# Kernel tuning notes

Measured on AMD Instinct MI355X. Metric: run time of the kernel, lower is better.

Reference implementation:

```python
import jax, jax.numpy as jnp
import numpy as np

B, S, H = 64, 512, 1024  # batch, seq_len, hidden (input_size == hidden_size per source)


def setup_inputs() -> dict:
    key = jax.random.key(0)
    k1, k2 = jax.random.split(key)
    x = jax.random.normal(k1, (B, S, H), dtype=jnp.float32)
    # xavier_uniform_ for U: bound = sqrt(6/(fan_in+fan_out))
    bound = float(np.sqrt(6.0 / (H + 4 * H)))
    U = jax.random.uniform(k2, (H, 4 * H), dtype=jnp.float32, minval=-bound, maxval=bound)
    bias = jnp.zeros((4 * H,), dtype=jnp.float32)
    return {"x": x, "U": U, "bias": bias}


def reference(x, U, bias):
    # Faithful LSTM recurrence (peephole=False; note: W is declared in the
    # original module but never used in forward, and the gate matmul uses U
    # on the input x_t, exactly as in the source).
    batch = x.shape[0]
    HS = U.shape[0]
    h0 = jnp.zeros((batch, HS), dtype=x.dtype)
    c0 = jnp.zeros((batch, HS), dtype=x.dtype)

    def step(carry, x_t):
        h_t, c_t = carry
        gates = x_t @ U + bias  # [B, 4H]
        i_t = jax.nn.sigmoid(gates[:, :HS])
        f_t = jax.nn.sigmoid(gates[:, HS:2 * HS])
        g_t = jnp.tanh(gates[:, 2 * HS:3 * HS])
        o_t = jax.nn.sigmoid(gates[:, 3 * HS:])
        c_t = f_t * c_t + i_t * g_t
        h_t = o_t * jnp.tanh(c_t)
        return (h_t, c_t), h_t

    (h_T, c_T), hs = jax.lax.scan(step, (h0, c0), jnp.swapaxes(x, 0, 1))  # hs: [S, B, H]
    hidden_sequence = jnp.swapaxes(hs, 0, 1)  # [B, S, H]
    return hidden_sequence, (h_T, c_T)
```

## Files before the change

kernel.cpp:

```cpp
#include <hip/hip_runtime.h>
#include <hip/hip_bf16.h>
#include <stdint.h>

typedef __bf16 bf16x8 __attribute__((ext_vector_type(8)));
typedef float  f32x4  __attribute__((ext_vector_type(4)));
typedef unsigned short u16x8 __attribute__((ext_vector_type(8)));
typedef unsigned short u16x4 __attribute__((ext_vector_type(4)));
typedef _Float16 f16x4 __attribute__((ext_vector_type(4)));

#define HS    1024
#define FOURH 4096
#define SEQ   512
#define BATCH 64

#define BAR()  asm volatile("s_barrier" ::: "memory")
#define VMW(n) asm volatile("s_waitcnt vmcnt(" #n ")" ::: "memory")

__device__ __forceinline__ unsigned short f2bf(float f) {
    unsigned u = __builtin_bit_cast(unsigned, f);
    u = (u + 0x7FFFu + ((u >> 16) & 1u)) >> 16;
    return (unsigned short)u;
}

__device__ __forceinline__ void gload_lds16(const void* g, void* l) {
    __builtin_amdgcn_global_load_lds(
        (const __attribute__((address_space(1))) void*)g,
        (__attribute__((address_space(3))) void*)l, 16, 0, 0);
}

__device__ __forceinline__ float fsigmoid(float v) {
    return __builtin_amdgcn_rcpf(1.f + __expf(-v));
}
__device__ __forceinline__ float ftanh(float v) {
    return 1.f - 2.f * __builtin_amdgcn_rcpf(1.f + __expf(2.f * v));
}

__global__ __launch_bounds__(256) void convert_x(const float* __restrict__ x,
                                                 unsigned short* __restrict__ xb,
                                                 long n8) {
    long i = (long)blockIdx.x * blockDim.x + threadIdx.x;
    long stride = (long)gridDim.x * blockDim.x;
    for (; i < n8; i += stride) {
        const float4* p = (const float4*)(x + i * 8);
        float4 a = p[0], b = p[1];
        u16x8 o;
        o[0] = f2bf(a.x); o[1] = f2bf(a.y); o[2] = f2bf(a.z); o[3] = f2bf(a.w);
        o[4] = f2bf(b.x); o[5] = f2bf(b.y); o[6] = f2bf(b.z); o[7] = f2bf(b.w);
        *(u16x8*)(xb + i * 8) = o;
    }
}

__global__ __launch_bounds__(256) void transpose_u(const float* __restrict__ U,
                                                   unsigned short* __restrict__ Ut) {
    __shared__ float tile[32][33];
    int bx = blockIdx.x;
    int tn = bx >> 5;
    int tk = bx & 31;
    int c = threadIdx.x & 31;
    int r = threadIdx.x >> 5;
#pragma unroll
    for (int i = 0; i < 4; ++i) {
        int k = tk * 32 + r + i * 8;
        tile[r + i * 8][c] = U[(size_t)k * FOURH + tn * 32 + c];
    }
    __syncthreads();
#pragma unroll
    for (int i = 0; i < 4; ++i) {
        int nl = r + i * 8;
        Ut[(size_t)(tn * 32 + nl) * HS + tk * 32 + c] = f2bf(tile[c][nl]);
    }
}

__global__ __launch_bounds__(512, 1) void gemm_gates8(
    const unsigned short* __restrict__ Xb,
    const unsigned short* __restrict__ Ut,
    const float* __restrict__ bias,
    _Float16* __restrict__ gates,
    int lg2chunk, int s0) {
    __shared__ unsigned short LDSU[65536];

    int nwg = gridDim.x;
    int bid = blockIdx.x;
    int wg = (bid & 7) * (nwg >> 3) + (bid >> 3);
    int mt = wg >> 4;
    int nt = wg & 15;

    int tid = threadIdx.x;
    int w = tid >> 6, l = tid & 63;
    int wr = w >> 2, wc = w & 3;
    int lr = l & 15, lg = l >> 4;

    const int m0 = mt * 256, n0 = nt * 256;
    const int cmask = (1 << lg2chunk) - 1;

    const int rdo = lr * 32 + ((lg * 8) ^ ((lr & 8) << 1));

    const int srow = l >> 2;
    const int skin = ((l & 3) * 8) ^ (((l >> 5) & 1) << 4);

    const unsigned short* pAq[4];
    const unsigned short* pBq[4];
#pragma unroll
    for (int q = 0; q < 4; ++q) {
        int rowg = q * 64 + (w >> 1) * 16 + srow;
        int mrow = m0 + rowg;
        int b = mrow >> lg2chunk, sl2 = mrow & cmask;
        pAq[q] = Xb + (size_t)(b * SEQ + s0 + sl2) * HS + (w & 1) * 32 + skin;
        pBq[q] = Ut + (size_t)(n0 + rowg) * HS + (w & 1) * 32 + skin;
    }
    const int dsub = (w >> 1) * 2 + (w & 1);

    f32x4 acc[8][4];
#pragma unroll
    for (int mi = 0; mi < 8; ++mi)
#pragma unroll
        for (int ni = 0; ni < 4; ++ni) acc[mi][ni] = 0.f;

#define SA(T, Q) gload_lds16(pAq[Q] + (T) * 64, \
        &LDSU[(((T) & 1) << 15) + ((Q) * 8 + dsub) * 512])
#define SB(T, Q) gload_lds16(pBq[Q] + (T) * 64, \
        &LDSU[(((T) & 1) << 15) + 16384 + ((Q) * 8 + dsub) * 512])

    bf16x8 aq[2][4], bn0[2][2], bn1[2][2];

#define RDA(MH) \
    _Pragma("unroll") for (int ks = 0; ks < 2; ++ks) \
    _Pragma("unroll") for (int mi = 0; mi < 4; ++mi) \
        aq[ks][mi] = *(const bf16x8*)(buf + ((wr * 8 + (MH) * 4 + mi) * 2 + ks) * 512 + rdo)
#define RDB(NH, BN) \
    _Pragma("unroll") for (int ks = 0; ks < 2; ++ks) \
    _Pragma("unroll") for (int ni = 0; ni < 2; ++ni) \
        BN[ks][ni] = *(const bf16x8*)(buf + 16384 + ((wc * 4 + (NH) * 2 + ni) * 2 + ks) * 512 + rdo)
#define MMQ(MH, NH, BN) \
    __builtin_amdgcn_s_setprio(1); \
    _Pragma("unroll") for (int ks = 0; ks < 2; ++ks) \
    _Pragma("unroll") for (int mi = 0; mi < 4; ++mi) \
    _Pragma("unroll") for (int ni = 0; ni < 2; ++ni) \
        acc[(MH) * 4 + mi][(NH) * 2 + ni] = __builtin_amdgcn_mfma_f32_16x16x32_bf16( \
            aq[ks][mi], BN[ks][ni], acc[(MH) * 4 + mi][(NH) * 2 + ni], 0, 0, 0); \
    __builtin_amdgcn_s_setprio(0)

    SA(0, 0); SA(0, 2); SB(0, 0); SB(0, 1); SB(0, 2); SB(0, 3); SA(0, 1); SA(0, 3);
    VMW(2); BAR();

    for (int t = 0; t < 16; ++t) {
        const unsigned short* buf = &LDSU[(t & 1) << 15];
        RDA(0);
        RDB(0, bn0);
        if (t < 15) { SA(t + 1, 0); SA(t + 1, 2); }
        MMQ(0, 0, bn0);
        RDB(1, bn1);
        if (t < 15) { SB(t + 1, 0); SB(t + 1, 1); SB(t + 1, 2); SB(t + 1, 3); }
        MMQ(0, 1, bn1);
        if (t < 15) { VMW(6); } else { VMW(0); }
        BAR();
        RDA(1);
        if (t < 15) { SA(t + 1, 1); SA(t + 1, 3); }
        MMQ(1, 1, bn1);
        MMQ(1, 0, bn0);
        if (t < 15) { VMW(2); }
        BAR();
    }

#pragma unroll
    for (int ni = 0; ni < 4; ++ni) {
        int gcol = n0 + wc * 64 + ni * 16 + lr;
        bool is_g = ((gcol >> 10) == 2);
        float bv = bias[gcol];
#pragma unroll
        for (int mi = 0; mi < 8; ++mi) {
            int rg = ((m0 + wr * 128 + mi * 16) >> 2) + lg;
            u16x4 pk;
#pragma unroll
            for (int r = 0; r < 4; ++r) {
                float v = acc[mi][ni][r] + bv;
                float e = is_g ? ftanh(v) : fsigmoid(v);
                pk[r] = __builtin_bit_cast(unsigned short, (_Float16)e);
            }
            *(u16x4*)(gates + ((size_t)rg * FOURH + gcol) * 4) = pk;
        }
    }
#undef SA
#undef SB
#undef RDA
#undef RDB
#undef MMQ
}

__global__ __launch_bounds__(256) void lstm_recur(
    const _Float16* __restrict__ gates,
    float* __restrict__ out,
    float* __restrict__ cstate,
    int chunk, int s0) {
    int t = blockIdx.x * 256 + threadIdx.x;
    int b = t >> 10, h = t & 1023;
    float c = (s0 == 0) ? 0.f : cstate[t];
    const _Float16* gp = gates + ((size_t)((b * chunk) >> 2) * FOURH + h) * 4;
    float* op = out + (size_t)(b * SEQ + s0) * HS + h;
    float hv = 0.f;
    const int ng = chunk >> 2;
    for (int g4 = 0; g4 < ng; g4 += 2) {
        f16x4 iv[2], fv[2], gv[2], ov[2];
#pragma unroll
        for (int u = 0; u < 2; ++u) {
            const _Float16* q = gp + (size_t)(g4 + u) * (FOURH * 4);
            iv[u] = *(const f16x4*)(q);
            fv[u] = *(const f16x4*)(q + 4096);
            gv[u] = *(const f16x4*)(q + 8192);
            ov[u] = *(const f16x4*)(q + 12288);
        }
#pragma unroll
        for (int u = 0; u < 2; ++u) {
#pragma unroll
            for (int r = 0; r < 4; ++r) {
                c = (float)fv[u][r] * c + (float)iv[u][r] * (float)gv[u][r];
                float th = ftanh(c);
                hv = (float)ov[u][r] * th;
                op[(size_t)((g4 + u) * 4 + r) * HS] = hv;
            }
        }
    }
    cstate[t] = c;
    if (s0 + chunk == SEQ) {
        out[(size_t)BATCH * SEQ * HS + t] = hv;
        out[(size_t)BATCH * SEQ * HS + BATCH * HS + t] = c;
    }
}

extern "C" void kernel_launch(void* const* d_in, const int* in_sizes, int n_in,
                              void* d_out, int out_size, void* d_ws, size_t ws_size,
                              hipStream_t stream) {
    const float* x    = (const float*)d_in[0];
    const float* U    = (const float*)d_in[1];
    const float* bias = (const float*)d_in[2];
    float* out = (float*)d_out;
    char*  ws  = (char*)d_ws;

    unsigned short* Xb = (unsigned short*)ws;
    unsigned short* Ut = (unsigned short*)(ws + 67108864);
    float* cstate      = (float*)(ws + 75497472);
    _Float16* gates    = (_Float16*)(ws + 75759616);
    const size_t fixed = 75759616;

    int chunk = 512;
    while (chunk > 4 && fixed + (size_t)BATCH * chunk * FOURH * 2 > ws_size)
        chunk >>= 1;
    int lg2 = 31 - __builtin_clz(chunk);

    convert_x<<<2048, 256, 0, stream>>>(x, Xb, (long)BATCH * SEQ * HS / 8);
    transpose_u<<<4096, 256, 0, stream>>>(U, Ut);

    for (int s0 = 0; s0 < SEQ; s0 += chunk) {
        int mtiles = (BATCH * chunk) / 256;
        gemm_gates8<<<mtiles * 16, 512, 0, stream>>>(Xb, Ut, bias, gates, lg2, s0);
        lstm_recur<<<256, 256, 0, stream>>>(gates, out, cstate, chunk, s0);
    }
}
```

Measured before the change: 401.3 us.

## Stage LSTM recurrence gate loads through double-buffered LDS with async copies

Adds a recurrence kernel that prefetches the next 16 timesteps of gate values into a double-buffered LDS region using direct global-to-LDS loads. The element-wise recurrence then reads from LDS while the next block streams in, hiding the global load latency along the serial time loop. The fallback kernel drops its two-step unrolled prefetch. The cost is extra barriers and 64KB of LDS per block, which limits occupancy.

```diff
diff --git a/kernel.cpp b/kernel.cpp
--- a/kernel.cpp
+++ b/kernel.cpp
@@ -94,7 +94,6 @@
     const int cmask = (1 << lg2chunk) - 1;
 
     const int rdo = lr * 32 + ((lg * 8) ^ ((lr & 8) << 1));
-
     const int srow = l >> 2;
     const int skin = ((l & 3) * 8) ^ (((l >> 5) & 1) << 4);
 
@@ -187,10 +186,74 @@
 #undef MMQ
 }
 
-__global__ __launch_bounds__(256) void lstm_recur(
+__global__ __launch_bounds__(256) void lstm_recur_lds(
     const _Float16* __restrict__ gates,
     float* __restrict__ out,
     float* __restrict__ cstate,
+    int chunk, int s0) {
+    __shared__ unsigned char LB[2][32768];
+
+    int tid = threadIdx.x;
+    int b = blockIdx.x >> 2;
+    int h0 = (blockIdx.x & 3) * 256;
+    int h = h0 + tid;
+    int tg = b * HS + h;
+
+    float c = (s0 == 0) ? 0.f : cstate[tg];
+    float hv = 0.f;
+    const size_t rgbase = (size_t)(b * chunk) >> 2;
+    const char* gbase = (const char*)gates;
+    float* op = out + (size_t)(b * SEQ + s0) * HS + h;
+
+    const int M = chunk >> 4;
+    const int wbase = (tid & 0xC0) * 16;
+
+    auto STAGE = [&](int m) {
+        unsigned char* dst0 = &LB[m & 1][0];
+        size_t rg0 = rgbase + (size_t)m * 4;
+#pragma unroll
+        for (int j = 0; j < 8; ++j) {
+            int q = j * 256 + tid;
+            int stripe = q >> 7;
+            int u = q & 127;
+            const char* src = gbase +
+                ((rg0 + (stripe >> 2)) * FOURH + (stripe & 3) * 1024 + h0 + u * 2) * 8;
+            gload_lds16(src, dst0 + j * 4096 + wbase);
+        }
+    };
+
+    STAGE(0);
+    for (int m = 0; m < M; ++m) {
+        if (m + 1 < M) { STAGE(m + 1); VMW(8); }
+        else           { VMW(0); }
+        BAR();
+        const unsigned char* sb = &LB[m & 1][0];
+#pragma unroll
+        for (int rg = 0; rg < 4; ++rg) {
+            f16x4 iv = *(const f16x4*)(sb + ((rg * 4 + 0) * 2048) + tid * 8);
+            f16x4 fv = *(const f16x4*)(sb + ((rg * 4 + 1) * 2048) + tid * 8);
+            f16x4 gv = *(const f16x4*)(sb + ((rg * 4 + 2) * 2048) + tid * 8);
+            f16x4 ov = *(const f16x4*)(sb + ((rg * 4 + 3) * 2048) + tid * 8);
+#pragma unroll
+            for (int r = 0; r < 4; ++r) {
+                c = (float)fv[r] * c + (float)iv[r] * (float)gv[r];
+                float th = ftanh(c);
+                hv = (float)ov[r] * th;
+                op[(size_t)(m * 16 + rg * 4 + r) * HS] = hv;
+            }
+        }
+        BAR();
+    }
+    cstate[tg] = c;
+    if (s0 + chunk == SEQ) {
+        out[(size_t)BATCH * SEQ * HS + tg] = hv;
+        out[(size_t)BATCH * SEQ * HS + BATCH * HS + tg] = c;
+    }
+}
+
+__global__ __launch_bounds__(256) void lstm_recur(
+    const _Float16* __restrict__ gates,
+    float* __restrict__ out, float* __restrict__ cstate,
     int chunk, int s0) {
     int t = blockIdx.x * 256 + threadIdx.x;
     int b = t >> 10, h = t & 1023;
@@ -199,25 +262,18 @@
     float* op = out + (size_t)(b * SEQ + s0) * HS + h;
     float hv = 0.f;
     const int ng = chunk >> 2;
-    for (int g4 = 0; g4 < ng; g4 += 2) {
-        f16x4 iv[2], fv[2], gv[2], ov[2];
-#pragma unroll
-        for (int u = 0; u < 2; ++u) {
-            const _Float16* q = gp + (size_t)(g4 + u) * (FOURH * 4);
-            iv[u] = *(const f16x4*)(q);
-            fv[u] = *(const f16x4*)(q + 4096);
-            gv[u] = *(const f16x4*)(q + 8192);
-            ov[u] = *(const f16x4*)(q + 12288);
-        }
-#pragma unroll
-        for (int u = 0; u < 2; ++u) {
-#pragma unroll
-            for (int r = 0; r < 4; ++r) {
-                c = (float)fv[u][r] * c + (float)iv[u][r] * (float)gv[u][r];
-                float th = ftanh(c);
-                hv = (float)ov[u][r] * th;
-                op[(size_t)((g4 + u) * 4 + r) * HS] = hv;
-            }
+    for (int g4 = 0; g4 < ng; ++g4) {
+        const _Float16* q = gp + (size_t)g4 * (FOURH * 4);
+        f16x4 iv = *(const f16x4*)(q);
+        f16x4 fv = *(const f16x4*)(q + 4096);
+        f16x4 gv = *(const f16x4*)(q + 8192);
+        f16x4 ov = *(const f16x4*)(q + 12288);
+#pragma unroll
+        for (int r = 0; r < 4; ++r) {
+            c = (float)fv[r] * c + (float)iv[r] * (float)gv[r];
+            float th = ftanh(c);
+            hv = (float)ov[r] * th;
+            op[(size_t)(g4 * 4 + r) * HS] = hv;
         }
     }
     cstate[t] = c;
@@ -253,6 +309,9 @@
     for (int s0 = 0; s0 < SEQ; s0 += chunk) {
         int mtiles = (BATCH * chunk) / 256;
         gemm_gates8<<<mtiles * 16, 512, 0, stream>>>(Xb, Ut, bias, gates, lg2, s0);
-        lstm_recur<<<256, 256, 0, stream>>>(gates, out, cstate, chunk, s0);
-    }
-}
+        if ((chunk & 15) == 0)
+            lstm_recur_lds<<<256, 256, 0, stream>>>(gates, out, cstate, chunk, s0);
+        else
+            lstm_recur<<<256, 256, 0, stream>>>(gates, out, cstate, chunk, s0);
+    }
+}
```

After: 400.5 us. Within noise of the previous version (-0.2%).

## Interleave U columns by gate so GEMM epilogue fuses i*g product

Applied to the files above, without the earlier changes.

The transposed weight rows are permuted so that each 16-column group of a wave holds the same hidden units across all four gates. The GEMM epilogue can then compute i*g, f and o together and store only three fp16 gate planes instead of four. This cuts the gate intermediate's write and read traffic by a quarter and lets a larger chunk fit in the workspace. The recurrence kernel reads the three planes and gains a remainder loop for odd group counts.

```diff
diff --git a/kernel.cpp b/kernel.cpp
--- a/kernel.cpp
+++ b/kernel.cpp
@@ -67,7 +67,10 @@
 #pragma unroll
     for (int i = 0; i < 4; ++i) {
         int nl = r + i * 8;
-        Ut[(size_t)(tn * 32 + nl) * HS + tk * 32 + c] = f2bf(tile[c][nl]);
+        int n = tn * 32 + nl;
+        int gate = n >> 10, h = n & 1023;
+        int pn = ((h >> 4) << 6) | (gate << 4) | (h & 15);
+        Ut[(size_t)pn * HS + tk * 32 + c] = f2bf(tile[c][nl]);
     }
 }
 
@@ -94,7 +97,6 @@
     const int cmask = (1 << lg2chunk) - 1;
 
     const int rdo = lr * 32 + ((lg * 8) ^ ((lr & 8) << 1));
-
     const int srow = l >> 2;
     const int skin = ((l & 3) * 8) ^ (((l >> 5) & 1) << 4);
 
@@ -162,23 +164,28 @@
         BAR();
     }
 
-#pragma unroll
-    for (int ni = 0; ni < 4; ++ni) {
-        int gcol = n0 + wc * 64 + ni * 16 + lr;
-        bool is_g = ((gcol >> 10) == 2);
-        float bv = bias[gcol];
-#pragma unroll
-        for (int mi = 0; mi < 8; ++mi) {
-            int rg = ((m0 + wr * 128 + mi * 16) >> 2) + lg;
-            u16x4 pk;
-#pragma unroll
-            for (int r = 0; r < 4; ++r) {
-                float v = acc[mi][ni][r] + bv;
-                float e = is_g ? ftanh(v) : fsigmoid(v);
-                pk[r] = __builtin_bit_cast(unsigned short, (_Float16)e);
-            }
-            *(u16x4*)(gates + ((size_t)rg * FOURH + gcol) * 4) = pk;
-        }
+    const int hh = ((n0 >> 6) + wc) * 16 + lr;
+    const float bi = bias[hh], bf = bias[1024 + hh];
+    const float bg = bias[2048 + hh], bo = bias[3072 + hh];
+#pragma unroll
+    for (int mi = 0; mi < 8; ++mi) {
+        size_t rg = (size_t)(((m0 + wr * 128 + mi * 16) >> 2) + lg);
+        u16x4 pkP, pkF, pkO;
+#pragma unroll
+        for (int r = 0; r < 4; ++r) {
+            float iv = fsigmoid(acc[mi][0][r] + bi);
+            float fv = fsigmoid(acc[mi][1][r] + bf);
+            float gv = ftanh(acc[mi][2][r] + bg);
+            float ov = fsigmoid(acc[mi][3][r] + bo);
+            float pv = iv * gv;
+            pkP[r] = __builtin_bit_cast(unsigned short, (_Float16)pv);
+            pkF[r] = __builtin_bit_cast(unsigned short, (_Float16)fv);
+            pkO[r] = __builtin_bit_cast(unsigned short, (_Float16)ov);
+        }
+        _Float16* gp = gates + rg * 12288 + hh * 4;
+        *(u16x4*)(gp)        = pkP;
+        *(u16x4*)(gp + 4096) = pkF;
+        *(u16x4*)(gp + 8192) = pkO;
     }
 #undef SA
 #undef SB
@@ -195,29 +202,42 @@
     int t = blockIdx.x * 256 + threadIdx.x;
     int b = t >> 10, h = t & 1023;
     float c = (s0 == 0) ? 0.f : cstate[t];
-    const _Float16* gp = gates + ((size_t)((b * chunk) >> 2) * FOURH + h) * 4;
+    const _Float16* gp = gates + (size_t)((b * chunk) >> 2) * 12288 + h * 4;
     float* op = out + (size_t)(b * SEQ + s0) * HS + h;
     float hv = 0.f;
     const int ng = chunk >> 2;
-    for (int g4 = 0; g4 < ng; g4 += 2) {
-        f16x4 iv[2], fv[2], gv[2], ov[2];
+    int g4 = 0;
+    for (; g4 + 1 < ng; g4 += 2) {
+        f16x4 pv[2], fv[2], ov[2];
 #pragma unroll
         for (int u = 0; u < 2; ++u) {
-            const _Float16* q = gp + (size_t)(g4 + u) * (FOURH * 4);
-            iv[u] = *(const f16x4*)(q);
+            const _Float16* q = gp + (size_t)(g4 + u) * 12288;
+            pv[u] = *(const f16x4*)(q);
             fv[u] = *(const f16x4*)(q + 4096);
-            gv[u] = *(const f16x4*)(q + 8192);
-            ov[u] = *(const f16x4*)(q + 12288);
+            ov[u] = *(const f16x4*)(q + 8192);
         }
 #pragma unroll
         for (int u = 0; u < 2; ++u) {
 #pragma unroll
             for (int r = 0; r < 4; ++r) {
-                c = (float)fv[u][r] * c + (float)iv[u][r] * (float)gv[u][r];
+                c = (float)fv[u][r] * c + (float)pv[u][r];
                 float th = ftanh(c);
                 hv = (float)ov[u][r] * th;
                 op[(size_t)((g4 + u) * 4 + r) * HS] = hv;
             }
+        }
+    }
+    for (; g4 < ng; ++g4) {
+        const _Float16* q = gp + (size_t)g4 * 12288;
+        f16x4 pv = *(const f16x4*)(q);
+        f16x4 fv = *(const f16x4*)(q + 4096);
+        f16x4 ov = *(const f16x4*)(q + 8192);
+#pragma unroll
+        for (int r = 0; r < 4; ++r) {
+            c = (float)fv[r] * c + (float)pv[r];
+            float th = ftanh(c);
+            hv = (float)ov[r] * th;
+            op[(size_t)(g4 * 4 + r) * HS] = hv;
         }
     }
     cstate[t] = c;
@@ -243,7 +263,7 @@
     const size_t fixed = 75759616;
 
     int chunk = 512;
-    while (chunk > 4 && fixed + (size_t)BATCH * chunk * FOURH * 2 > ws_size)
+    while (chunk > 4 && fixed + (size_t)BATCH * chunk * 6144 > ws_size)
         chunk >>= 1;
     int lg2 = 31 - __builtin_clz(chunk);
 
```

Result: faster. 376.7 us, median of 2 (-6.1%).
